# Kernel tuning notes

Measured on AMD Instinct MI355X. Metric: run time of the kernel, lower is better.

The kernel has to match this reference:

```python
import jax, jax.numpy as jnp
import numpy as np

DIM = 1024
E = 8
HID = 4 * DIM  # DomainExpert FFN hidden size


def setup_inputs() -> dict:
    key = jax.random.key(0)
    ks = jax.random.split(key, 7)
    x = jax.random.normal(ks[0], (1, 2048, DIM), dtype=jnp.float32)
    Wr = jax.random.normal(ks[1], (DIM, E), dtype=jnp.float32) * (DIM ** -0.5)
    br = jnp.zeros((E,), dtype=jnp.float32)
    W1 = jax.random.normal(ks[2], (E, DIM, HID), dtype=jnp.float32) * (DIM ** -0.5)
    b1 = jnp.zeros((E, 1, HID), dtype=jnp.float32)
    W2 = jax.random.normal(ks[3], (E, HID, DIM), dtype=jnp.float32) * (HID ** -0.5)
    b2 = jnp.zeros((E, 1, DIM), dtype=jnp.float32)
    return {"x": x, "Wr": Wr, "br": br, "W1": W1, "b1": b1, "W2": W2, "b2": b2}


def reference(x, Wr, br, W1, b1, W2, b2):
    B, T, D = x.shape
    flat = x.reshape(B * T, D)                       # [N, D]
    logits = flat @ Wr + br                          # [N, E]
    z_loss = jnp.mean(jax.nn.logsumexp(logits, axis=-1) ** 2)
    probs = jax.nn.softmax(logits, axis=-1)          # eval path (no Gumbel)
    top_p, top_i = jax.lax.top_k(probs, 2)           # [N, 2]
    top_p = top_p / (top_p.sum(-1, keepdims=True) + 1e-12)
    N = flat.shape[0]
    nE = Wr.shape[1]
    # combine weights: w[t, e] = renormalized top-2 prob if e selected, else 0
    w = jnp.zeros((N, nE), dtype=flat.dtype).at[
        jnp.arange(N)[:, None], top_i].add(top_p)   # [N, E]
    # dense (jit-friendly) expert compute; combine masks out unselected experts
    h = jax.nn.gelu(jnp.einsum('td,edh->teh', flat, W1) + b1.transpose(1, 0, 2))  # [N, E, HID]
    y = jnp.einsum('teh,ehd->ted', h, W2) + b2.transpose(1, 0, 2)                 # [N, E, D]
    out = jnp.einsum('ted,te->td', y, w).reshape(B, T, D)
    importance = probs.mean(axis=0)                                               # [E]
    fi = jax.nn.one_hot(top_i, nE, dtype=flat.dtype).sum(axis=1).mean(axis=0)     # [E]
    aux_loss = jnp.asarray(nE, flat.dtype) * (importance * fi).sum()
    return out, z_loss, aux_loss
```

## Files before the change

kernel.cpp:

```cpp
#include <hip/hip_runtime.h>
#include <math.h>

#define N_TOK 2048
#define DIM   1024
#define NEXP  8
#define HID   4096
#define TOTPAIR (2 * N_TOK)

#define BM 128
#define BN 128
#define BK 32
#define KSPLIT2 4

typedef __bf16 bf16x8 __attribute__((ext_vector_type(8)));
typedef __bf16 bf16x4 __attribute__((ext_vector_type(4)));
typedef float  f32x4  __attribute__((ext_vector_type(4)));

__device__ __forceinline__ float gelu_tanh(float v) {
    float a = 0.7978845608028654f * (v + 0.044715f * v * v * v);
    a = fminf(fmaxf(a, -15.f), 15.f);
    float t = __expf(-2.f * a);
    return 0.5f * v * (1.f + (1.f - t) / (1.f + t));
}

__device__ __forceinline__ void stage16(const __bf16* g, __bf16* lds_base, int lane) {
#if defined(__has_builtin) && __has_builtin(__builtin_amdgcn_global_load_lds)
    __builtin_amdgcn_global_load_lds((const __attribute__((address_space(1))) void*)g,
                                     (__attribute__((address_space(3))) void*)lds_base,
                                     16, 0, 0);
#else
    *(bf16x8*)((char*)lds_base + (size_t)lane * 16) = *(const bf16x8*)g;
#endif
}

__device__ __forceinline__ int expert_prefix(const int* cnt, int e) {
    int s = 0;
    for (int i = 0; i < NEXP; i++) s += (i < e) ? cnt[i] : 0;
    return s;
}

__device__ __forceinline__ void router_body(
    int t, int lane,
    const float* __restrict__ x, const float* __restrict__ Wr, const float* __restrict__ br,
    float* __restrict__ probs, float* __restrict__ lsq,
    int* __restrict__ cnt, int* __restrict__ tok, float* __restrict__ wl) {
    const float* xr = x + (size_t)t * DIM;
    float acc[NEXP];
#pragma unroll
    for (int e = 0; e < NEXP; e++) acc[e] = 0.f;
    for (int d = lane; d < DIM; d += 64) {
        float xv = xr[d];
        const float* wr = Wr + (size_t)d * NEXP;
#pragma unroll
        for (int e = 0; e < NEXP; e++) acc[e] = fmaf(xv, wr[e], acc[e]);
    }
#pragma unroll
    for (int off = 32; off >= 1; off >>= 1) {
#pragma unroll
        for (int e = 0; e < NEXP; e++) acc[e] += __shfl_xor(acc[e], off, 64);
    }
    if (lane == 0) {
        float lg[NEXP], mx = -1e30f;
#pragma unroll
        for (int e = 0; e < NEXP; e++) { lg[e] = acc[e] + br[e]; mx = fmaxf(mx, lg[e]); }
        float se = 0.f, p[NEXP];
#pragma unroll
        for (int e = 0; e < NEXP; e++) { p[e] = expf(lg[e] - mx); se += p[e]; }
        float inv = 1.f / se;
        float lse = mx + logf(se);
        lsq[t] = lse * lse;
#pragma unroll
        for (int e = 0; e < NEXP; e++) probs[t * NEXP + e] = p[e] * inv;
        int i0 = 0;
#pragma unroll
        for (int e = 1; e < NEXP; e++) if (p[e] > p[i0]) i0 = e;
        int i1 = (i0 == 0) ? 1 : 0;
#pragma unroll
        for (int e = 0; e < NEXP; e++) if (e != i0 && p[e] > p[i1]) i1 = e;
        float p0 = p[i0] * inv, p1 = p[i1] * inv;
        float rn = 1.f / (p0 + p1 + 1e-12f);
        int pos0 = atomicAdd(&cnt[i0], 1);
        tok[i0 * N_TOK + pos0] = t;
        wl[i0 * N_TOK + pos0] = p0 * rn;
        int pos1 = atomicAdd(&cnt[i1], 1);
        tok[i1 * N_TOK + pos1] = t;
        wl[i1 * N_TOK + pos1] = p1 * rn;
    }
}

__global__ void router_kernel(const float* __restrict__ x, const float* __restrict__ Wr,
                              const float* __restrict__ br,
                              float* __restrict__ probs, float* __restrict__ lsq,
                              int* __restrict__ cnt, int* __restrict__ tok,
                              float* __restrict__ wl) {
    router_body(blockIdx.x, threadIdx.x, x, Wr, br, probs, lsq, cnt, tok, wl);
}

__global__ __launch_bounds__(256) void prep_kernel(
    const float* __restrict__ x, const float* __restrict__ Wr, const float* __restrict__ br,
    float* __restrict__ probs, float* __restrict__ lsq,
    int* __restrict__ cnt, int* __restrict__ tok, float* __restrict__ wl,
    __bf16* __restrict__ xb) {
    const int b = blockIdx.x;
    const int tid = threadIdx.x;
    if (b < 512) {
        int t = b * 4 + (tid >> 6);
        router_body(t, tid & 63, x, Wr, br, probs, lsq, cnt, tok, wl);
        return;
    }
    int idx = (b - 512) * 256 + tid;
    float4 v = ((const float4*)x)[idx];
    bf16x4 o;
    o.x = (__bf16)v.x; o.y = (__bf16)v.y; o.z = (__bf16)v.z; o.w = (__bf16)v.w;
    ((bf16x4*)xb)[idx] = o;
}

__global__ __launch_bounds__(256, 4) void gemm1_kernel(
    const __bf16* __restrict__ xb, const float* __restrict__ W1,
    const float* __restrict__ b1,
    const int* __restrict__ cnt,
    const int* __restrict__ tok, __bf16* __restrict__ h) {
    const int e = blockIdx.z;
    const int ce = cnt[e];
    const int mstart = blockIdx.y * BM;
    if (mstart >= ce) return;
    const int n0 = blockIdx.x * BN;
    const int offe = expert_prefix(cnt, e);

    __shared__ __bf16 smem[BM * 128];
    __shared__ int toksh[BM];
    __bf16* As = smem;
    __bf16* Bs = smem + 4096;

    const int tid = threadIdx.x;
    if (tid < BM) {
        int idx = mstart + tid;
        toksh[tid] = (idx < ce) ? tok[e * N_TOK + idx] : 0;
    }
    __syncthreads();

    const int lane = tid & 63;
    const int wid  = tid >> 6;
    const int row0 = (wid >> 1) * 64;
    const int col0 = (wid & 1) * 64;
    const int quad = lane >> 4;
    const int lcol = lane & 15;

    const int sub = lane >> 2;
    const int gk  = (((lane & 3) ^ (sub & 3)) << 3);
    const int ra0 = wid * 32 + sub;
    const int ra1 = ra0 + 16;
    const __bf16* pA0 = xb + (size_t)toksh[ra0] * DIM + gk;
    const __bf16* pA1 = xb + (size_t)toksh[ra1] * DIM + gk;
    __bf16* lA0 = &As[(wid * 2 + 0) * 512];
    __bf16* lA1 = &As[(wid * 2 + 1) * 512];

    const int khalf = (wid >> 1) * 16;
    const int nl    = (wid & 1) * 64 + lane;
    const float* __restrict__ W1e = W1 + (size_t)e * DIM * HID;
    const float* wsrc = W1e + (size_t)khalf * HID + n0 + nl;

    const int aswz = (quad ^ (lcol & 3)) << 3;
    const __bf16* aF = &As[(row0 + lcol) * BK + aswz];

    f32x4 acc[4][4];
#pragma unroll
    for (int i = 0; i < 4; i++)
#pragma unroll
        for (int j = 0; j < 4; j++) acc[i][j] = (f32x4){0.f, 0.f, 0.f, 0.f};

    for (int k0 = 0; k0 < DIM; k0 += BK) {
        float v[16];
        const float* ws = wsrc + (size_t)k0 * HID;
#pragma unroll
        for (int j = 0; j < 16; j++) v[j] = ws[(size_t)j * HID];
        stage16(pA0 + k0, lA0, lane);
        stage16(pA1 + k0, lA1, lane);
#pragma unroll
        for (int q = 0; q < 4; q++) {
            bf16x4 pk;
            pk.x = (__bf16)v[q * 4 + 0]; pk.y = (__bf16)v[q * 4 + 1];
            pk.z = (__bf16)v[q * 4 + 2]; pk.w = (__bf16)v[q * 4 + 3];
            int c = (wid >> 1) * 2 + (q >> 1);
            int slot = c ^ (nl & 3);
            *(bf16x4*)&Bs[slot * 1024 + nl * 8 + (q & 1) * 4] = pk;
        }
        __syncthreads();
        bf16x8 af[4], bfr[4];
#pragma unroll
        for (int i = 0; i < 4; i++) af[i]  = *(const bf16x8*)(aF + i * 16 * BK);
#pragma unroll
        for (int j = 0; j < 4; j++)
            bfr[j] = *(const bf16x8*)&Bs[((quad ^ (lcol & 3)) * 1024) + (col0 + j * 16 + lcol) * 8];
#pragma unroll
        for (int i = 0; i < 4; i++)
#pragma unroll
            for (int j = 0; j < 4; j++)
                acc[i][j] = __builtin_amdgcn_mfma_f32_16x16x32_bf16(af[i], bfr[j], acc[i][j], 0, 0, 0);
        __syncthreads();
    }

    const float* __restrict__ b1e = b1 + (size_t)e * HID;
    float bj[4];
#pragma unroll
    for (int j = 0; j < 4; j++) bj[j] = b1e[n0 + col0 + j * 16 + lcol];
#pragma unroll
    for (int i = 0; i < 4; i++)
#pragma unroll
        for (int reg = 0; reg < 4; reg++) {
            int row = row0 + i * 16 + quad * 4 + reg;
#pragma unroll
            for (int j = 0; j < 4; j++) {
                int col = col0 + j * 16 + lcol;
                int slot = (col >> 3) ^ (row & 15);
                smem[row * 128 + slot * 8 + (col & 7)] =
                    (__bf16)gelu_tanh(acc[i][j][reg] + bj[j]);
            }
        }
    __syncthreads();
    {
        int row = tid >> 1, half = tid & 1;
        int pos = mstart + row;
        if (pos < ce) {
            __bf16* hp = h + (size_t)(offe + pos) * HID + n0 + half * 64;
#pragma unroll
            for (int j = 0; j < 8; j++) {
                int chunk = half * 8 + j;
                int slot = chunk ^ (row & 15);
                *(bf16x8*)(hp + j * 8) = *(const bf16x8*)&smem[row * 128 + slot * 8];
            }
        }
    }
}

__global__ __launch_bounds__(256, 4) void gemm2_kernel(
    const __bf16* __restrict__ h, const float* __restrict__ W2,
    const float* __restrict__ b2,
    const int* __restrict__ cnt,
    const int* __restrict__ tok, const float* __restrict__ wl,
    float* __restrict__ out) {
    const int e = blockIdx.z >> 2;
    const int split = blockIdx.z & 3;
    const int ce = cnt[e];
    const int mstart = blockIdx.y * BM;
    if (mstart >= ce) return;
    const int n0 = blockIdx.x * BN;
    const int ks = split * (HID / KSPLIT2);
    const int offe = expert_prefix(cnt, e);

    __shared__ __bf16 As[BM * BK];
    __shared__ __bf16 Bs[4 * 128 * 8];
    __shared__ int   toksh[BM];
    __shared__ float wsh[BM];

    const int tid = threadIdx.x;
    if (tid < BM) {
        int idx = mstart + tid;
        toksh[tid] = (idx < ce) ? tok[e * N_TOK + idx] : 0;
        wsh[tid]   = (idx < ce) ? wl[e * N_TOK + idx] : 0.f;
    }
    __syncthreads();

    const int lane = tid & 63;
    const int wid  = tid >> 6;
    const int row0 = (wid >> 1) * 64;
    const int col0 = (wid & 1) * 64;
    const int quad = lane >> 4;
    const int lcol = lane & 15;

    const int sub = lane >> 2;
    const int gk  = (((lane & 3) ^ (sub & 3)) << 3);
    const int ra0 = wid * 32 + sub;
    const int ra1 = ra0 + 16;
    int hr0 = offe + mstart + ra0; if (hr0 >= TOTPAIR) hr0 = TOTPAIR - 1;
    int hr1 = offe + mstart + ra1; if (hr1 >= TOTPAIR) hr1 = TOTPAIR - 1;
    const __bf16* pA0 = h + (size_t)hr0 * HID + ks + gk;
    const __bf16* pA1 = h + (size_t)hr1 * HID + ks + gk;
    __bf16* lA0 = &As[(wid * 2 + 0) * 512];
    __bf16* lA1 = &As[(wid * 2 + 1) * 512];

    const int khalf = (wid >> 1) * 16;
    const int nl    = (wid & 1) * 64 + lane;
    const float* __restrict__ W2e = W2 + (size_t)e * HID * DIM;
    const float* wsrc = W2e + (size_t)(ks + khalf) * DIM + n0 + nl;

    const int aswz = (quad ^ (lcol & 3)) << 3;
    const __bf16* aF = &As[(row0 + lcol) * BK + aswz];

    f32x4 acc[4][4];
#pragma unroll
    for (int i = 0; i < 4; i++)
#pragma unroll
        for (int j = 0; j < 4; j++) acc[i][j] = (f32x4){0.f, 0.f, 0.f, 0.f};

    for (int k0 = 0; k0 < HID / KSPLIT2; k0 += BK) {
        float v[16];
        const float* ws = wsrc + (size_t)k0 * DIM;
#pragma unroll
        for (int j = 0; j < 16; j++) v[j] = ws[(size_t)j * DIM];
        stage16(pA0 + k0, lA0, lane);
        stage16(pA1 + k0, lA1, lane);
#pragma unroll
        for (int q = 0; q < 4; q++) {
            bf16x4 pk;
            pk.x = (__bf16)v[q * 4 + 0]; pk.y = (__bf16)v[q * 4 + 1];
            pk.z = (__bf16)v[q * 4 + 2]; pk.w = (__bf16)v[q * 4 + 3];
            int c = (wid >> 1) * 2 + (q >> 1);
            int slot = c ^ (nl & 3);
            *(bf16x4*)&Bs[slot * 1024 + nl * 8 + (q & 1) * 4] = pk;
        }
        __syncthreads();
        bf16x8 af[4], bfr[4];
#pragma unroll
        for (int i = 0; i < 4; i++) af[i]  = *(const bf16x8*)(aF + i * 16 * BK);
#pragma unroll
        for (int j = 0; j < 4; j++)
            bfr[j] = *(const bf16x8*)&Bs[((quad ^ (lcol & 3)) * 1024) + (col0 + j * 16 + lcol) * 8];
#pragma unroll
        for (int i = 0; i < 4; i++)
#pragma unroll
            for (int j = 0; j < 4; j++)
                acc[i][j] = __builtin_amdgcn_mfma_f32_16x16x32_bf16(af[i], bfr[j], acc[i][j], 0, 0, 0);
        __syncthreads();
    }

    const float* __restrict__ b2e = b2 + (size_t)e * DIM;
    const bool addBias = (split == 0);
#pragma unroll
    for (int i = 0; i < 4; i++) {
#pragma unroll
        for (int reg = 0; reg < 4; reg++) {
            int lrow = row0 + i * 16 + quad * 4 + reg;
            int pos = mstart + lrow;
            if (pos >= ce) continue;
            int tokm = toksh[lrow];
            float w = wsh[lrow];
#pragma unroll
            for (int j = 0; j < 4; j++) {
                int gcol = n0 + col0 + j * 16 + lcol;
                float vv = acc[i][j][reg] + (addBias ? b2e[gcol] : 0.f);
                atomicAdd(&out[(size_t)tokm * DIM + gcol], w * vv);
            }
        }
    }
}

__global__ __launch_bounds__(256, 2) void ffn_fallback_kernel(
    const float* __restrict__ x,
    const float* __restrict__ W1, const float* __restrict__ b1,
    const float* __restrict__ W2, const float* __restrict__ b2,
    const int* __restrict__ cnt, const int* __restrict__ tok,
    const float* __restrict__ wl, float* __restrict__ out) {
    const int e = blockIdx.y;
    const int ce = cnt[e];
    const int start = blockIdx.x * 16;
    if (start >= ce) return;
    __shared__ float hs[16][128];
    __shared__ int toks[16];
    __shared__ float wgt[16];
    const int tid = threadIdx.x;
    if (tid < 16) {
        int idx = start + tid;
        if (idx < ce) { toks[tid] = tok[e * N_TOK + idx]; wgt[tid] = wl[e * N_TOK + idx]; }
        else          { toks[tid] = -1;                   wgt[tid] = 0.f; }
    }
    __syncthreads();
    const float* __restrict__ W1e = W1 + (size_t)e * DIM * HID;
    const float* __restrict__ W2e = W2 + (size_t)e * HID * DIM;
    const int am  = tid >> 4;
    const int aj0 = (tid & 15) * 8;
    const int at  = toks[am];
    const float* __restrict__ xrow = x + (size_t)(at < 0 ? 0 : at) * DIM;
    const int n0 = tid * 4;
    float acc[16][4];
#pragma unroll
    for (int m = 0; m < 16; m++)
#pragma unroll
        for (int i = 0; i < 4; i++) acc[m][i] = 0.f;
    for (int c = 0; c < HID; c += 128) {
        float ha[8];
#pragma unroll
        for (int r = 0; r < 8; r++) ha[r] = 0.f;
        const float* wp = W1e + c + aj0;
        for (int d = 0; d < DIM; d += 4) {
            float4 xv = *(const float4*)(xrow + d);
#pragma unroll
            for (int k = 0; k < 4; k++) {
                const float* wr = wp + (size_t)(d + k) * HID;
                float4 wa = *(const float4*)(wr);
                float4 wb = *(const float4*)(wr + 4);
                float xk = (k == 0) ? xv.x : (k == 1) ? xv.y : (k == 2) ? xv.z : xv.w;
                ha[0] = fmaf(xk, wa.x, ha[0]); ha[1] = fmaf(xk, wa.y, ha[1]);
                ha[2] = fmaf(xk, wa.z, ha[2]); ha[3] = fmaf(xk, wa.w, ha[3]);
                ha[4] = fmaf(xk, wb.x, ha[4]); ha[5] = fmaf(xk, wb.y, ha[5]);
                ha[6] = fmaf(xk, wb.z, ha[6]); ha[7] = fmaf(xk, wb.w, ha[7]);
            }
        }
        __syncthreads();
#pragma unroll
        for (int r = 0; r < 8; r++) {
            float v = ha[r] + b1[e * HID + c + aj0 + r];
            hs[am][aj0 + r] = gelu_tanh(v);
        }
        __syncthreads();
        for (int jj = 0; jj < 128; jj++) {
            float4 wv = *(const float4*)(W2e + (size_t)(c + jj) * DIM + n0);
#pragma unroll
            for (int m = 0; m < 16; m++) {
                float hv = hs[m][jj];
                acc[m][0] = fmaf(hv, wv.x, acc[m][0]); acc[m][1] = fmaf(hv, wv.y, acc[m][1]);
                acc[m][2] = fmaf(hv, wv.z, acc[m][2]); acc[m][3] = fmaf(hv, wv.w, acc[m][3]);
            }
        }
    }
    const float* bp = b2 + e * DIM + n0;
    float b0 = bp[0], b1v = bp[1], b2v = bp[2], b3 = bp[3];
#pragma unroll 1
    for (int m = 0; m < 16; m++) {
        int t = toks[m];
        if (t < 0) continue;
        float w = wgt[m];
        float* op = out + (size_t)t * DIM + n0;
        atomicAdd(op + 0, w * (acc[m][0] + b0));
        atomicAdd(op + 1, w * (acc[m][1] + b1v));
        atomicAdd(op + 2, w * (acc[m][2] + b2v));
        atomicAdd(op + 3, w * (acc[m][3] + b3));
    }
}

__global__ void finalize_kernel(const float* __restrict__ probs, const float* __restrict__ lsq,
                                const int* __restrict__ cnt, float* __restrict__ scal) {
    __shared__ float part[256][9];
    const int tid = threadIdx.x;
    float z = 0.f;
    float im[NEXP];
#pragma unroll
    for (int e = 0; e < NEXP; e++) im[e] = 0.f;
    for (int t = tid; t < N_TOK; t += 256) {
        z += lsq[t];
#pragma unroll
        for (int e = 0; e < NEXP; e++) im[e] += probs[t * NEXP + e];
    }
    part[tid][0] = z;
#pragma unroll
    for (int e = 0; e < NEXP; e++) part[tid][1 + e] = im[e];
    __syncthreads();
    if (tid == 0) {
        float zs = 0.f, ims[NEXP];
        for (int e = 0; e < NEXP; e++) ims[e] = 0.f;
        for (int i = 0; i < 256; i++) {
            zs += part[i][0];
            for (int e = 0; e < NEXP; e++) ims[e] += part[i][1 + e];
        }
        float nInv = 1.0f / (float)N_TOK;
        float aux = 0.f;
        for (int e = 0; e < NEXP; e++) aux += (ims[e] * nInv) * ((float)cnt[e] * nInv);
        scal[0] = zs * nInv;
        scal[1] = (float)NEXP * aux;
    }
}

extern "C" void kernel_launch(void* const* d_in, const int* in_sizes, int n_in,
                              void* d_out, int out_size, void* d_ws, size_t ws_size,
                              hipStream_t stream) {
    const float* x  = (const float*)d_in[0];
    const float* Wr = (const float*)d_in[1];
    const float* br = (const float*)d_in[2];
    const float* W1 = (const float*)d_in[3];
    const float* b1 = (const float*)d_in[4];
    const float* W2 = (const float*)d_in[5];
    const float* b2 = (const float*)d_in[6];
    float* out = (float*)d_out;

    char* base = (char*)d_ws;
    int*   cnt   = (int*)(base);
    int*   tokp  = (int*)(base + 64);
    float* wlp   = (float*)(base + 64 + 65536);
    float* probs = (float*)(base + 64 + 2 * 65536);
    float* lsq   = (float*)(base + 64 + 3 * 65536);
    const size_t SMALL_END = 64 + 3 * 65536 + 8192;
    __bf16* xb   = (__bf16*)(base + SMALL_END);
    __bf16* hbuf = (__bf16*)(base + SMALL_END + 4194304ull);
    const size_t REQ = SMALL_END + 4194304ull + 33554432ull;

    hipMemsetAsync(base, 0, 64, stream);
    hipMemsetAsync(d_out, 0, (size_t)out_size * sizeof(float), stream);

    if (ws_size >= REQ) {
        prep_kernel<<<512 + 2048, 256, 0, stream>>>(
            x, Wr, br, probs, lsq, cnt, tokp, wlp, xb);
        gemm1_kernel<<<dim3(HID / BN, N_TOK / BM, NEXP), 256, 0, stream>>>(
            xb, W1, b1, cnt, tokp, hbuf);
        gemm2_kernel<<<dim3(DIM / BN, N_TOK / BM, NEXP * KSPLIT2), 256, 0, stream>>>(
            hbuf, W2, b2, cnt, tokp, wlp, out);
    } else {
        router_kernel<<<N_TOK, 64, 0, stream>>>(x, Wr, br, probs, lsq, cnt, tokp, wlp);
        ffn_fallback_kernel<<<dim3(128, NEXP), 256, 0, stream>>>(
            x, W1, b1, W2, b2, cnt, tokp, wlp, out);
    }

    finalize_kernel<<<1, 256, 0, stream>>>(probs, lsq, cnt, out + (size_t)N_TOK * DIM);
}
```

Baseline: 540.1 us.

## Double-buffer LDS in expert GEMMs and compact grid to occupied expert tiles

Both expert GEMM kernels now prefetch the next K-tile's weights into registers and the next activation tile into a second LDS buffer while computing on the current one, needing one barrier per iteration instead of two. The launch grid is compacted to a flat slot index that maps onto only the occupied (expert, M-tile) pairs, removing thousands of early-exit blocks. The trade-off is doubled LDS use (notably in gemm2) and more registers held live, which may reduce occupancy.

Result: no change. 546.3 us (+1.1%).

```diff
diff --git a/kernel.cpp b/kernel.cpp
--- a/kernel.cpp
+++ b/kernel.cpp
@@ -11,6 +11,7 @@
 #define BN 128
 #define BK 32
 #define KSPLIT2 4
+#define MAXSLOT 40
 
 typedef __bf16 bf16x8 __attribute__((ext_vector_type(8)));
 typedef __bf16 bf16x4 __attribute__((ext_vector_type(4)));
@@ -37,6 +38,18 @@
     int s = 0;
     for (int i = 0; i < NEXP; i++) s += (i < e) ? cnt[i] : 0;
     return s;
+}
+
+__device__ __forceinline__ bool slot_to_em(const int* __restrict__ cnt,
+                                           int slot, int& e, int& m, int& ce) {
+    int s = slot;
+    for (int i = 0; i < NEXP; i++) {
+        int c = cnt[i];
+        int t = (c + BM - 1) >> 7;
+        if (s < t) { e = i; m = s; ce = c; return true; }
+        s -= t;
+    }
+    return false;
 }
 
 __device__ __forceinline__ void router_body(
@@ -120,17 +133,14 @@
     const float* __restrict__ b1,
     const int* __restrict__ cnt,
     const int* __restrict__ tok, __bf16* __restrict__ h) {
-    const int e = blockIdx.z;
-    const int ce = cnt[e];
-    const int mstart = blockIdx.y * BM;
-    if (mstart >= ce) return;
-    const int n0 = blockIdx.x * BN;
+    int e, m, ce;
+    if (!slot_to_em(cnt, blockIdx.x >> 5, e, m, ce)) return;
+    const int mstart = m * BM;
+    const int n0 = (blockIdx.x & 31) * BN;
     const int offe = expert_prefix(cnt, e);
 
-    __shared__ __bf16 smem[BM * 128];
+    __shared__ __bf16 smem[16384];
     __shared__ int toksh[BM];
-    __bf16* As = smem;
-    __bf16* Bs = smem + 4096;
 
     const int tid = threadIdx.x;
     if (tid < BM) {
@@ -152,16 +162,19 @@
     const int ra1 = ra0 + 16;
     const __bf16* pA0 = xb + (size_t)toksh[ra0] * DIM + gk;
     const __bf16* pA1 = xb + (size_t)toksh[ra1] * DIM + gk;
-    __bf16* lA0 = &As[(wid * 2 + 0) * 512];
-    __bf16* lA1 = &As[(wid * 2 + 1) * 512];
+    const int lAoff0 = (wid * 2 + 0) * 512;
+    const int lAoff1 = (wid * 2 + 1) * 512;
 
     const int khalf = (wid >> 1) * 16;
     const int nl    = (wid & 1) * 64 + lane;
     const float* __restrict__ W1e = W1 + (size_t)e * DIM * HID;
     const float* wsrc = W1e + (size_t)khalf * HID + n0 + nl;
+    const int bslot0 = ((wid >> 1) * 2 + 0) ^ (nl & 3);
+    const int bslot1 = ((wid >> 1) * 2 + 1) ^ (nl & 3);
 
     const int aswz = (quad ^ (lcol & 3)) << 3;
-    const __bf16* aF = &As[(row0 + lcol) * BK + aswz];
+    const int aFo  = (row0 + lcol) * BK + aswz;
+    const int bCh  = (quad ^ (lcol & 3)) * 1024;
 
     f32x4 acc[4][4];
 #pragma unroll
@@ -169,34 +182,57 @@
 #pragma unroll
         for (int j = 0; j < 4; j++) acc[i][j] = (f32x4){0.f, 0.f, 0.f, 0.f};
 
-    for (int k0 = 0; k0 < DIM; k0 += BK) {
+    {
         float v[16];
-        const float* ws = wsrc + (size_t)k0 * HID;
-#pragma unroll
-        for (int j = 0; j < 16; j++) v[j] = ws[(size_t)j * HID];
-        stage16(pA0 + k0, lA0, lane);
-        stage16(pA1 + k0, lA1, lane);
+#pragma unroll
+        for (int j = 0; j < 16; j++) v[j] = wsrc[(size_t)j * HID];
+        stage16(pA0, &smem[lAoff0], lane);
+        stage16(pA1, &smem[lAoff1], lane);
 #pragma unroll
         for (int q = 0; q < 4; q++) {
             bf16x4 pk;
             pk.x = (__bf16)v[q * 4 + 0]; pk.y = (__bf16)v[q * 4 + 1];
             pk.z = (__bf16)v[q * 4 + 2]; pk.w = (__bf16)v[q * 4 + 3];
-            int c = (wid >> 1) * 2 + (q >> 1);
-            int slot = c ^ (nl & 3);
-            *(bf16x4*)&Bs[slot * 1024 + nl * 8 + (q & 1) * 4] = pk;
-        }
-        __syncthreads();
+            int slot = (q >> 1) ? bslot1 : bslot0;
+            *(bf16x4*)&smem[8192 + slot * 1024 + nl * 8 + (q & 1) * 4] = pk;
+        }
+    }
+    __syncthreads();
+
+    const int NK = DIM / BK;
+    for (int k = 0; k < NK; k++) {
+        const int cur = k & 1, nxt = cur ^ 1;
+        const bool more = (k + 1 < NK);
+        float v[16];
+        if (more) {
+            const float* ws = wsrc + (size_t)((k + 1) * BK) * HID;
+#pragma unroll
+            for (int j = 0; j < 16; j++) v[j] = ws[(size_t)j * HID];
+            stage16(pA0 + (k + 1) * BK, &smem[nxt * 4096 + lAoff0], lane);
+            stage16(pA1 + (k + 1) * BK, &smem[nxt * 4096 + lAoff1], lane);
+        }
         bf16x8 af[4], bfr[4];
 #pragma unroll
-        for (int i = 0; i < 4; i++) af[i]  = *(const bf16x8*)(aF + i * 16 * BK);
+        for (int i = 0; i < 4; i++)
+            af[i] = *(const bf16x8*)&smem[cur * 4096 + aFo + i * 16 * BK];
 #pragma unroll
         for (int j = 0; j < 4; j++)
-            bfr[j] = *(const bf16x8*)&Bs[((quad ^ (lcol & 3)) * 1024) + (col0 + j * 16 + lcol) * 8];
+            bfr[j] = *(const bf16x8*)&smem[8192 + cur * 4096 + bCh + (col0 + j * 16 + lcol) * 8];
 #pragma unroll
         for (int i = 0; i < 4; i++)
 #pragma unroll
             for (int j = 0; j < 4; j++)
                 acc[i][j] = __builtin_amdgcn_mfma_f32_16x16x32_bf16(af[i], bfr[j], acc[i][j], 0, 0, 0);
+        if (more) {
+#pragma unroll
+            for (int q = 0; q < 4; q++) {
+                bf16x4 pk;
+                pk.x = (__bf16)v[q * 4 + 0]; pk.y = (__bf16)v[q * 4 + 1];
+                pk.z = (__bf16)v[q * 4 + 2]; pk.w = (__bf16)v[q * 4 + 3];
+                int slot = (q >> 1) ? bslot1 : bslot0;
+                *(bf16x4*)&smem[8192 + nxt * 4096 + slot * 1024 + nl * 8 + (q & 1) * 4] = pk;
+            }
+        }
         __syncthreads();
     }
 
@@ -239,17 +275,16 @@
     const int* __restrict__ cnt,
     const int* __restrict__ tok, const float* __restrict__ wl,
     float* __restrict__ out) {
-    const int e = blockIdx.z >> 2;
-    const int split = blockIdx.z & 3;
-    const int ce = cnt[e];
-    const int mstart = blockIdx.y * BM;
-    if (mstart >= ce) return;
-    const int n0 = blockIdx.x * BN;
+    int e, m, ce;
+    if (!slot_to_em(cnt, blockIdx.x >> 5, e, m, ce)) return;
+    const int inner = blockIdx.x & 31;
+    const int n0 = (inner & 7) * BN;
+    const int split = inner >> 3;
+    const int mstart = m * BM;
     const int ks = split * (HID / KSPLIT2);
     const int offe = expert_prefix(cnt, e);
 
-    __shared__ __bf16 As[BM * BK];
-    __shared__ __bf16 Bs[4 * 128 * 8];
+    __shared__ __bf16 smem[16384];
     __shared__ int   toksh[BM];
     __shared__ float wsh[BM];
 
@@ -276,16 +311,19 @@
     int hr1 = offe + mstart + ra1; if (hr1 >= TOTPAIR) hr1 = TOTPAIR - 1;
     const __bf16* pA0 = h + (size_t)hr0 * HID + ks + gk;
     const __bf16* pA1 = h + (size_t)hr1 * HID + ks + gk;
-    __bf16* lA0 = &As[(wid * 2 + 0) * 512];
-    __bf16* lA1 = &As[(wid * 2 + 1) * 512];
+    const int lAoff0 = (wid * 2 + 0) * 512;
+    const int lAoff1 = (wid * 2 + 1) * 512;
 
     const int khalf = (wid >> 1) * 16;
     const int nl    = (wid & 1) * 64 + lane;
     const float* __restrict__ W2e = W2 + (size_t)e * HID * DIM;
     const float* wsrc = W2e + (size_t)(ks + khalf) * DIM + n0 + nl;
+    const int bslot0 = ((wid >> 1) * 2 + 0) ^ (nl & 3);
+    const int bslot1 = ((wid >> 1) * 2 + 1) ^ (nl & 3);
 
     const int aswz = (quad ^ (lcol & 3)) << 3;
-    const __bf16* aF = &As[(row0 + lcol) * BK + aswz];
+    const int aFo  = (row0 + lcol) * BK + aswz;
+    const int bCh  = (quad ^ (lcol & 3)) * 1024;
 
     f32x4 acc[4][4];
 #pragma unroll
@@ -293,34 +331,57 @@
 #pragma unroll
         for (int j = 0; j < 4; j++) acc[i][j] = (f32x4){0.f, 0.f, 0.f, 0.f};
 
-    for (int k0 = 0; k0 < HID / KSPLIT2; k0 += BK) {
+    {
         float v[16];
-        const float* ws = wsrc + (size_t)k0 * DIM;
-#pragma unroll
-        for (int j = 0; j < 16; j++) v[j] = ws[(size_t)j * DIM];
-        stage16(pA0 + k0, lA0, lane);
-        stage16(pA1 + k0, lA1, lane);
+#pragma unroll
+        for (int j = 0; j < 16; j++) v[j] = wsrc[(size_t)j * DIM];
+        stage16(pA0, &smem[lAoff0], lane);
+        stage16(pA1, &smem[lAoff1], lane);
 #pragma unroll
         for (int q = 0; q < 4; q++) {
             bf16x4 pk;
             pk.x = (__bf16)v[q * 4 + 0]; pk.y = (__bf16)v[q * 4 + 1];
             pk.z = (__bf16)v[q * 4 + 2]; pk.w = (__bf16)v[q * 4 + 3];
-            int c = (wid >> 1) * 2 + (q >> 1);
-            int slot = c ^ (nl & 3);
-            *(bf16x4*)&Bs[slot * 1024 + nl * 8 + (q & 1) * 4] = pk;
-        }
-        __syncthreads();
+            int slot = (q >> 1) ? bslot1 : bslot0;
+            *(bf16x4*)&smem[8192 + slot * 1024 + nl * 8 + (q & 1) * 4] = pk;
+        }
+    }
+    __syncthreads();
+
+    const int NK = (HID / KSPLIT2) / BK;
+    for (int k = 0; k < NK; k++) {
+        const int cur = k & 1, nxt = cur ^ 1;
+        const bool more = (k + 1 < NK);
+        float v[16];
+        if (more) {
+            const float* ws = wsrc + (size_t)((k + 1) * BK) * DIM;
+#pragma unroll
+            for (int j = 0; j < 16; j++) v[j] = ws[(size_t)j * DIM];
+            stage16(pA0 + (k + 1) * BK, &smem[nxt * 4096 + lAoff0], lane);
+            stage16(pA1 + (k + 1) * BK, &smem[nxt * 4096 + lAoff1], lane);
+        }
         bf16x8 af[4], bfr[4];
 #pragma unroll
-        for (int i = 0; i < 4; i++) af[i]  = *(const bf16x8*)(aF + i * 16 * BK);
+        for (int i = 0; i < 4; i++)
+            af[i] = *(const bf16x8*)&smem[cur * 4096 + aFo + i * 16 * BK];
 #pragma unroll
         for (int j = 0; j < 4; j++)
-            bfr[j] = *(const bf16x8*)&Bs[((quad ^ (lcol & 3)) * 1024) + (col0 + j * 16 + lcol) * 8];
+            bfr[j] = *(const bf16x8*)&smem[8192 + cur * 4096 + bCh + (col0 + j * 16 + lcol) * 8];
 #pragma unroll
         for (int i = 0; i < 4; i++)
 #pragma unroll
             for (int j = 0; j < 4; j++)
                 acc[i][j] = __builtin_amdgcn_mfma_f32_16x16x32_bf16(af[i], bfr[j], acc[i][j], 0, 0, 0);
+        if (more) {
+#pragma unroll
+            for (int q = 0; q < 4; q++) {
+                bf16x4 pk;
+                pk.x = (__bf16)v[q * 4 + 0]; pk.y = (__bf16)v[q * 4 + 1];
+                pk.z = (__bf16)v[q * 4 + 2]; pk.w = (__bf16)v[q * 4 + 3];
+                int slot = (q >> 1) ? bslot1 : bslot0;
+                *(bf16x4*)&smem[8192 + nxt * 4096 + slot * 1024 + nl * 8 + (q & 1) * 4] = pk;
+            }
+        }
         __syncthreads();
     }
 
@@ -489,9 +550,9 @@
     if (ws_size >= REQ) {
         prep_kernel<<<512 + 2048, 256, 0, stream>>>(
             x, Wr, br, probs, lsq, cnt, tokp, wlp, xb);
-        gemm1_kernel<<<dim3(HID / BN, N_TOK / BM, NEXP), 256, 0, stream>>>(
+        gemm1_kernel<<<MAXSLOT * 32, 256, 0, stream>>>(
             xb, W1, b1, cnt, tokp, hbuf);
-        gemm2_kernel<<<dim3(DIM / BN, N_TOK / BM, NEXP * KSPLIT2), 256, 0, stream>>>(
+        gemm2_kernel<<<MAXSLOT * 32, 256, 0, stream>>>(
             hbuf, W2, b2, cnt, tokp, wlp, out);
     } else {
         router_kernel<<<N_TOK, 64, 0, stream>>>(x, Wr, br, probs, lsq, cnt, tokp, wlp);
```
